# Kernel tuning notes

Measured on AMD Instinct MI355X. Metric: run time of the kernel, lower is better.

## Reference

```python
import jax, jax.numpy as jnp
import numpy as np

N_NODES = 50000
N_EDGES = 600000
NUM_GRAPHS = 64


def gcn_conv(x, W, b, src, dst, n):
    # PyG GCNConv: x' = D^{-1/2} (A + I) D^{-1/2} (x W) + b, self-loops implicit
    h = x @ W  # [N, H]
    deg = jax.ops.segment_sum(jnp.ones((src.shape[0],), h.dtype), dst, num_segments=n) + 1.0
    dinv = jax.lax.rsqrt(deg)  # [N]
    norm = dinv[src] * dinv[dst]  # [E]
    msg = h[src] * norm[:, None]  # [E, H] gather + scale
    agg = jax.ops.segment_sum(msg, dst, num_segments=n)  # scatter-add
    agg = agg + h * (dinv * dinv)[:, None]  # self-loop contribution
    return agg + b


def global_mean_pool(x, batch, num_graphs):
    s = jax.ops.segment_sum(x, batch, num_segments=num_graphs)
    cnt = jax.ops.segment_sum(jnp.ones((x.shape[0],), x.dtype), batch, num_segments=num_graphs)
    return s / jnp.maximum(cnt, 1.0)[:, None]


def setup_inputs() -> dict:
    key = jax.random.key(0)
    ks = jax.random.split(key, 12)
    x = jax.random.normal(ks[0], (N_NODES, 128), jnp.float32)
    edge_index = jax.random.randint(ks[1], (2, N_EDGES), 0, N_NODES, jnp.int64)
    batch = jnp.sort(jax.random.randint(ks[2], (N_NODES,), 0, NUM_GRAPHS, jnp.int64))
    W1 = jax.random.normal(ks[3], (128, 128), jnp.float32) * 0.08
    b1 = jax.random.normal(ks[4], (128,), jnp.float32) * 0.02
    W2 = jax.random.normal(ks[5], (128, 128), jnp.float32) * 0.08
    b2 = jax.random.normal(ks[6], (128,), jnp.float32) * 0.02
    Wfc1 = jax.random.normal(ks[7], (128, 64), jnp.float32) * 0.08
    bfc1 = jax.random.normal(ks[8], (64,), jnp.float32) * 0.02
    Wfc2 = jax.random.normal(ks[9], (64, 1), jnp.float32) * 0.08
    bfc2 = jax.random.normal(ks[10], (1,), jnp.float32) * 0.02
    return {"x": x, "edge_index": edge_index, "batch": batch,
            "W1": W1, "b1": b1, "W2": W2, "b2": b2,
            "Wfc1": Wfc1, "bfc1": bfc1, "Wfc2": Wfc2, "bfc2": bfc2}


def reference(x, edge_index, batch, W1, b1, W2, b2, Wfc1, bfc1, Wfc2, bfc2):
    n = x.shape[0]
    src, dst = edge_index[0], edge_index[1]
    h = jax.nn.relu(gcn_conv(x, W1, b1, src, dst, n))
    # dropout = identity (eval mode)
    h = jax.nn.relu(gcn_conv(h, W2, b2, src, dst, n))
    g = global_mean_pool(h, batch, NUM_GRAPHS)  # [G, H]
    g = jax.nn.relu(g @ Wfc1 + bfc1)
    return g @ Wfc2 + bfc2  # [G, 1]
```

## Files before the change

kernel.cpp:

```cpp
#include <hip/hip_runtime.h>
#include <hip/hip_fp16.h>


#define ELLK 40

typedef short bf16x8 __attribute__((ext_vector_type(8)));
typedef float f32x4  __attribute__((ext_vector_type(4)));

__device__ inline unsigned short f2bf_rne(float f) {
    unsigned u = __float_as_uint(f);
    unsigned r = (u + 0x7fffu + ((u >> 16) & 1u)) >> 16;
    return (unsigned short)r;
}
__device__ inline float bf2f(unsigned short h) {
    return __uint_as_float(((unsigned)h) << 16);
}

__global__ __launch_bounds__(256) void wconv_zero(const float* __restrict__ W1,
                                                  const float* __restrict__ W2,
                                                  unsigned short* __restrict__ W1h,
                                                  unsigned short* __restrict__ W1l,
                                                  unsigned short* __restrict__ W2h,
                                                  unsigned short* __restrict__ W2l,
                                                  int* __restrict__ count,
                                                  float* __restrict__ pooled,
                                                  float* __restrict__ cnt, int N) {
    int tid = threadIdx.x;
    int b = blockIdx.x;
    if (b < 128) {
        int i = b * 256 + tid;
        const float* W = (i < 16384) ? W1 : W2;
        unsigned short* Wh = (i < 16384) ? W1h : W2h;
        unsigned short* Wl = (i < 16384) ? W1l : W2l;
        int ii = i & 16383;
        int k = ii >> 7, n = ii & 127;
        float v = W[ii];
        unsigned short h = f2bf_rne(v);
        float lo = v - bf2f(h);
        int ct = n >> 4, nn = n & 15, ks = k >> 5, q = (k >> 3) & 3, j = k & 7;
        int oidx = (((ct * 4 + ks) * 64) + (q * 16 + nn)) * 8 + j;
        Wh[oidx] = h;
        Wl[oidx] = f2bf_rne(lo);
    } else {
        int idx = (b - 128) * 256 + tid;
        if (idx < N) count[idx] = 0;
        else if (idx < N + 8192) pooled[idx - N] = 0.f;
        else if (idx < N + 8256) cnt[idx - N - 8192] = 0.f;
    }
}

template <bool RELU_IN>
__device__ __forceinline__ void gemm_body(const float* __restrict__ X,
                                          const unsigned short* __restrict__ Wfh,
                                          const unsigned short* __restrict__ Wfl,
                                          __half* __restrict__ OUT, int M, int blk) {
    __shared__ unsigned short Xh[64][136];
    __shared__ unsigned short Xl[64][136];
    int tid = threadIdx.x;
    int w = tid >> 6, l = tid & 63;
    int m0 = blk * 64;

#pragma unroll
    for (int it = 0; it < 8; it++) {
        int i = tid + it * 256;
        int row = i >> 5, c4 = i & 31;
        int grow = m0 + row;
        float4 v = make_float4(0.f, 0.f, 0.f, 0.f);
        if (grow < M) v = *(const float4*)(X + (size_t)grow * 128 + c4 * 4);
        if (RELU_IN) {
            v.x = fmaxf(v.x, 0.f); v.y = fmaxf(v.y, 0.f);
            v.z = fmaxf(v.z, 0.f); v.w = fmaxf(v.w, 0.f);
        }
        float a[4] = {v.x, v.y, v.z, v.w};
        ushort4 hi, lo;
        unsigned short* hp = (unsigned short*)&hi;
        unsigned short* lp = (unsigned short*)&lo;
#pragma unroll
        for (int e = 0; e < 4; e++) {
            unsigned short h = f2bf_rne(a[e]);
            hp[e] = h;
            lp[e] = f2bf_rne(a[e] - bf2f(h));
        }
        *(ushort4*)&Xh[row][c4 * 4] = hi;
        *(ushort4*)&Xl[row][c4 * 4] = lo;
    }
    __syncthreads();

    int q = l >> 4, nn = l & 15;
    f32x4 acc[8];
#pragma unroll
    for (int ct = 0; ct < 8; ct++) acc[ct] = (f32x4){0.f, 0.f, 0.f, 0.f};

#pragma unroll
    for (int ks = 0; ks < 4; ks++) {
        bf16x8 ahi = *(const bf16x8*)&Xh[w * 16 + nn][ks * 32 + q * 8];
        bf16x8 alo = *(const bf16x8*)&Xl[w * 16 + nn][ks * 32 + q * 8];
#pragma unroll
        for (int ct = 0; ct < 8; ct++) {
            size_t fo = ((size_t)(ct * 4 + ks) * 64 + l) * 8;
            bf16x8 bhi = *(const bf16x8*)(Wfh + fo);
            bf16x8 blo = *(const bf16x8*)(Wfl + fo);
            acc[ct] = __builtin_amdgcn_mfma_f32_16x16x32_bf16(ahi, bhi, acc[ct], 0, 0, 0);
            acc[ct] = __builtin_amdgcn_mfma_f32_16x16x32_bf16(alo, bhi, acc[ct], 0, 0, 0);
            acc[ct] = __builtin_amdgcn_mfma_f32_16x16x32_bf16(ahi, blo, acc[ct], 0, 0, 0);
        }
    }
    __syncthreads();

#pragma unroll
    for (int r = 0; r < 4; r++) {
        int lrow = w * 16 + q * 4 + r;
#pragma unroll
        for (int ct = 0; ct < 8; ct++) {
            __half hv = __float2half(acc[ct][r]);
            Xh[lrow][ct * 16 + nn] = __half_as_ushort(hv);
        }
    }
    __syncthreads();
#pragma unroll
    for (int t = 0; t < 4; t++) {
        int c = tid + t * 256;
        int row = c >> 4, seg = c & 15;
        int grow = m0 + row;
        if (grow < M) {
            uint4 v = *(uint4*)&Xh[row][seg * 8];
            *(uint4*)((unsigned short*)OUT + (size_t)grow * 128 + seg * 8) = v;
        }
    }
}

__global__ __launch_bounds__(256) void gemm_mfma_relu(const float* __restrict__ X,
                                                      const unsigned short* __restrict__ Wfh,
                                                      const unsigned short* __restrict__ Wfl,
                                                      __half* __restrict__ OUT, int M) {
    gemm_body<true>(X, Wfh, Wfl, OUT, M, blockIdx.x);
}

__global__ __launch_bounds__(256) void fused_hg(const float* __restrict__ X,
                                                const unsigned short* __restrict__ Wfh,
                                                const unsigned short* __restrict__ Wfl,
                                                __half* __restrict__ OUT, int M, int gblocks,
                                                const int* __restrict__ dst,
                                                int* __restrict__ count,
                                                unsigned short* __restrict__ rank, int E) {
    if ((int)blockIdx.x < gblocks) {
        gemm_body<false>(X, Wfh, Wfl, OUT, M, blockIdx.x);
    } else {
        int e = ((int)blockIdx.x - gblocks) * 256 + (int)threadIdx.x;
        if (e < E) {
            int d = dst[e];
            rank[e] = (unsigned short)atomicAdd(&count[d], 1);
        }
    }
}

__global__ void scatter_norm(const int* __restrict__ src, const int* __restrict__ dst,
                             const unsigned short* __restrict__ rank,
                             const int* __restrict__ count,
                             int2* __restrict__ ell, int E) {
    int e = blockIdx.x * blockDim.x + threadIdx.x;
    if (e < E) {
        int s = src[e], d = dst[e];
        int r = rank[e];
        float ds = 1.0f / sqrtf((float)count[s] + 1.0f);
        float dd = 1.0f / sqrtf((float)count[d] + 1.0f);
        if (r < ELLK) ell[(size_t)d * ELLK + r] = make_int2(s, __float_as_int(ds * dd));
    }
}

__global__ __launch_bounds__(256) void gather_ell(const __half* __restrict__ h,
                                                  const float* __restrict__ bias,
                                                  const int* __restrict__ count,
                                                  const long long* __restrict__ ell,
                                                  float* __restrict__ B, int N) {
    int n = blockIdx.x * 4 + (threadIdx.x >> 6);
    int lane = threadIdx.x & 63;
    if (n >= N) return;
    int sub = lane >> 4, cl = lane & 15;
    int cn = count[n];
    int cnl = min(cn, ELLK);
    float din = 1.0f / sqrtf((float)cn + 1.0f);
    const unsigned short* hb = (const unsigned short*)h;
    const long long* row = ell + (size_t)n * ELLK;

    float a0 = 0.f, a1 = 0.f, a2 = 0.f, a3 = 0.f;
    float a4 = 0.f, a5 = 0.f, a6 = 0.f, a7 = 0.f;

    if (sub == 0) {
        float sw = din * din;
        uint4 raw = *(const uint4*)(hb + (size_t)n * 128 + cl * 8);
        const __half2* hh = (const __half2*)&raw;
        float2 f0 = __half22float2(hh[0]);
        float2 f1 = __half22float2(hh[1]);
        float2 f2 = __half22float2(hh[2]);
        float2 f3 = __half22float2(hh[3]);
        a0 = fmaf(f0.x, sw, a0); a1 = fmaf(f0.y, sw, a1);
        a2 = fmaf(f1.x, sw, a2); a3 = fmaf(f1.y, sw, a3);
        a4 = fmaf(f2.x, sw, a4); a5 = fmaf(f2.y, sw, a5);
        a6 = fmaf(f3.x, sw, a6); a7 = fmaf(f3.y, sw, a7);
    }

    for (int base = 0; base < cnl; base += 32) {
        int e1 = cnl - 1;
        long long v[8];
#pragma unroll
        for (int k = 0; k < 8; k++) {
            int j = base + sub + k * 4;
            v[k] = row[min(j, e1)];
        }
        float nr[8];
#pragma unroll
        for (int k = 0; k < 8; k++) {
            int j = base + sub + k * 4;
            nr[k] = (j < cnl) ? __int_as_float((int)(v[k] >> 32)) : 0.f;
        }
        uint4 r[8];
#pragma unroll
        for (int k = 0; k < 8; k++)
            r[k] = *(const uint4*)(hb + (size_t)(int)v[k] * 128 + cl * 8);
#pragma unroll
        for (int k = 0; k < 8; k++) {
            const __half2* hh = (const __half2*)&r[k];
            float2 f0 = __half22float2(hh[0]), f1 = __half22float2(hh[1]);
            float2 f2 = __half22float2(hh[2]), f3 = __half22float2(hh[3]);
            a0 = fmaf(f0.x, nr[k], a0); a1 = fmaf(f0.y, nr[k], a1);
            a2 = fmaf(f1.x, nr[k], a2); a3 = fmaf(f1.y, nr[k], a3);
            a4 = fmaf(f2.x, nr[k], a4); a5 = fmaf(f2.y, nr[k], a5);
            a6 = fmaf(f3.x, nr[k], a6); a7 = fmaf(f3.y, nr[k], a7);
        }
    }

#pragma unroll
    for (int m = 16; m < 64; m <<= 1) {
        a0 += __shfl_xor(a0, m, 64); a1 += __shfl_xor(a1, m, 64);
        a2 += __shfl_xor(a2, m, 64); a3 += __shfl_xor(a3, m, 64);
        a4 += __shfl_xor(a4, m, 64); a5 += __shfl_xor(a5, m, 64);
        a6 += __shfl_xor(a6, m, 64); a7 += __shfl_xor(a7, m, 64);
    }

    if (sub == 0) {
        float4 o0, o1;
        o0.x = a0 + bias[cl * 8 + 0]; o0.y = a1 + bias[cl * 8 + 1];
        o0.z = a2 + bias[cl * 8 + 2]; o0.w = a3 + bias[cl * 8 + 3];
        o1.x = a4 + bias[cl * 8 + 4]; o1.y = a5 + bias[cl * 8 + 5];
        o1.z = a6 + bias[cl * 8 + 6]; o1.w = a7 + bias[cl * 8 + 7];
        *(float4*)(B + (size_t)n * 128 + cl * 8) = o0;
        *(float4*)(B + (size_t)n * 128 + cl * 8 + 4) = o1;
    }
}

__global__ __launch_bounds__(256) void pool_kernel(const float* __restrict__ B,
                                                   const int* __restrict__ batch,
                                                   float* pooled, float* cnt, int N) {
    int c = threadIdx.x & 127;
    int half = threadIdx.x >> 7;
    int n0 = blockIdx.x * 128;
    float acc = 0.f, cacc = 0.f;
    int curg = -1;
    for (int i = half; i < 128; i += 2) {
        int n = n0 + i;
        if (n >= N) break;
        int g = batch[n];
        float v = fmaxf(B[(size_t)n * 128 + c], 0.f);
        if (g != curg) {
            if (curg >= 0) {
                atomicAdd(&pooled[curg * 128 + c], acc);
                if (c == 0) atomicAdd(&cnt[curg], cacc);
            }
            curg = g; acc = 0.f; cacc = 0.f;
        }
        acc += v; cacc += 1.f;
    }
    if (curg >= 0) {
        atomicAdd(&pooled[curg * 128 + c], acc);
        if (c == 0) atomicAdd(&cnt[curg], cacc);
    }
}

__global__ __launch_bounds__(64) void head_kernel(const float* __restrict__ pooled,
                                                  const float* __restrict__ cnt,
                                                  const float* __restrict__ Wfc1,
                                                  const float* __restrict__ bfc1,
                                                  const float* __restrict__ Wfc2,
                                                  const float* __restrict__ bfc2,
                                                  float* __restrict__ out) {
    __shared__ float mean[128];
    int g = blockIdx.x;
    int t = threadIdx.x;
    float inv = 1.0f / fmaxf(cnt[g], 1.0f);
    mean[t] = pooled[g * 128 + t] * inv;
    mean[t + 64] = pooled[g * 128 + t + 64] * inv;
    __syncthreads();
    float s = bfc1[t];
#pragma unroll 4
    for (int k = 0; k < 128; k++) s = fmaf(mean[k], Wfc1[k * 64 + t], s);
    float p = fmaxf(s, 0.f) * Wfc2[t];
#pragma unroll
    for (int o = 32; o > 0; o >>= 1) p += __shfl_down(p, o, 64);
    if (t == 0) out[g] = p + bfc2[0];
}

extern "C" void kernel_launch(void* const* d_in, const int* in_sizes, int n_in,
                              void* d_out, int out_size, void* d_ws, size_t ws_size,
                              hipStream_t stream) {
    const float* x    = (const float*)d_in[0];
    const int*   edge = (const int*)d_in[1];
    const int*   batch= (const int*)d_in[2];
    const float* W1   = (const float*)d_in[3];
    const float* b1   = (const float*)d_in[4];
    const float* W2   = (const float*)d_in[5];
    const float* b2   = (const float*)d_in[6];
    const float* Wfc1 = (const float*)d_in[7];
    const float* bfc1 = (const float*)d_in[8];
    const float* Wfc2 = (const float*)d_in[9];
    const float* bfc2 = (const float*)d_in[10];
    float* out = (float*)d_out;

    int N = in_sizes[0] / 128;
    int E = in_sizes[1] / 2;
    const int* src = edge;
    const int* dst = edge + E;

    char* ws = (char*)d_ws;
    size_t off = 0;
    auto alloc = [&](size_t bytes) { void* p = ws + off; off += (bytes + 255) & ~(size_t)255; return p; };
    __half* Ah    = (__half*)alloc((size_t)N * 128 * sizeof(__half));
    float* B      = (float*)alloc((size_t)N * 128 * sizeof(float));
    int*   count  = (int*)alloc((size_t)N * sizeof(int));
    unsigned short* rank = (unsigned short*)alloc((size_t)E * sizeof(unsigned short));
    int2*  ell    = (int2*)alloc((size_t)N * ELLK * sizeof(int2));
    float* pooled = (float*)alloc(64 * 128 * sizeof(float));
    float* cnt    = (float*)alloc(64 * sizeof(float));
    unsigned short* W1h = (unsigned short*)alloc(16384 * sizeof(short));
    unsigned short* W1l = (unsigned short*)alloc(16384 * sizeof(short));
    unsigned short* W2h = (unsigned short*)alloc(16384 * sizeof(short));
    unsigned short* W2l = (unsigned short*)alloc(16384 * sizeof(short));

    int hb = (E + 255) / 256;
    int gblocks = (N + 63) / 64;
    int ablocks = (N + 3) / 4;
    int zb = (N + 8256 + 255) / 256;

    wconv_zero<<<128 + zb, 256, 0, stream>>>(W1, W2, W1h, W1l, W2h, W2l,
                                             count, pooled, cnt, N);

    fused_hg<<<gblocks + hb, 256, 0, stream>>>(x, W1h, W1l, Ah, N, gblocks,
                                               dst, count, rank, E);

    scatter_norm<<<hb, 256, 0, stream>>>(src, dst, rank, count, ell, E);

    gather_ell<<<ablocks, 256, 0, stream>>>(Ah, b1, count, (const long long*)ell, B, N);

    gemm_mfma_relu<<<gblocks, 256, 0, stream>>>(B, W2h, W2l, Ah, N);

    gather_ell<<<ablocks, 256, 0, stream>>>(Ah, b2, count, (const long long*)ell, B, N);

    pool_kernel<<<(N + 127) / 128, 256, 0, stream>>>(B, batch, pooled, cnt, N);
    head_kernel<<<64, 64, 0, stream>>>(pooled, cnt, Wfc1, bfc1, Wfc2, bfc2, out);
}
```

Before: 259.2 us.

## Fuse layer-1 aggregation with layer-2 GEMM and layer-2 aggregation with pooling

Replaces four kernels (gather, relu-GEMM, gather, pool) with two. The first applies bias and ReLU to the aggregated rows, splits them into bf16 hi/lo halves in shared memory and runs the MFMA GEMM in the same block. The second aggregates and mean-pools from shared memory. This drops the fp32 intermediate buffer round trips through HBM and two launches. In exchange, the gather unroll falls from 8 to 4 edges per subgroup, which lowers memory-level parallelism, and the 512-thread blocks use more shared memory, which can lower occupancy.

```diff
diff --git a/kernel.cpp b/kernel.cpp
--- a/kernel.cpp
+++ b/kernel.cpp
@@ -129,13 +129,6 @@
     }
 }
 
-__global__ __launch_bounds__(256) void gemm_mfma_relu(const float* __restrict__ X,
-                                                      const unsigned short* __restrict__ Wfh,
-                                                      const unsigned short* __restrict__ Wfl,
-                                                      __half* __restrict__ OUT, int M) {
-    gemm_body<true>(X, Wfh, Wfl, OUT, M, blockIdx.x);
-}
-
 __global__ __launch_bounds__(256) void fused_hg(const float* __restrict__ X,
                                                 const unsigned short* __restrict__ Wfh,
                                                 const unsigned short* __restrict__ Wfl,
@@ -168,100 +161,208 @@
     }
 }
 
-__global__ __launch_bounds__(256) void gather_ell(const __half* __restrict__ h,
-                                                  const float* __restrict__ bias,
-                                                  const int* __restrict__ count,
-                                                  const long long* __restrict__ ell,
-                                                  float* __restrict__ B, int N) {
-    int n = blockIdx.x * 4 + (threadIdx.x >> 6);
-    int lane = threadIdx.x & 63;
-    if (n >= N) return;
-    int sub = lane >> 4, cl = lane & 15;
+__device__ __forceinline__ void gather_node(const unsigned short* __restrict__ hb,
+                                            const long long* __restrict__ ell,
+                                            const int* __restrict__ count,
+                                            int n, int sub, int cl, float a[8]) {
     int cn = count[n];
     int cnl = min(cn, ELLK);
     float din = 1.0f / sqrtf((float)cn + 1.0f);
-    const unsigned short* hb = (const unsigned short*)h;
     const long long* row = ell + (size_t)n * ELLK;
-
-    float a0 = 0.f, a1 = 0.f, a2 = 0.f, a3 = 0.f;
-    float a4 = 0.f, a5 = 0.f, a6 = 0.f, a7 = 0.f;
-
     if (sub == 0) {
         float sw = din * din;
         uint4 raw = *(const uint4*)(hb + (size_t)n * 128 + cl * 8);
         const __half2* hh = (const __half2*)&raw;
-        float2 f0 = __half22float2(hh[0]);
-        float2 f1 = __half22float2(hh[1]);
-        float2 f2 = __half22float2(hh[2]);
-        float2 f3 = __half22float2(hh[3]);
-        a0 = fmaf(f0.x, sw, a0); a1 = fmaf(f0.y, sw, a1);
-        a2 = fmaf(f1.x, sw, a2); a3 = fmaf(f1.y, sw, a3);
-        a4 = fmaf(f2.x, sw, a4); a5 = fmaf(f2.y, sw, a5);
-        a6 = fmaf(f3.x, sw, a6); a7 = fmaf(f3.y, sw, a7);
-    }
-
-    for (int base = 0; base < cnl; base += 32) {
+        float2 f0 = __half22float2(hh[0]), f1 = __half22float2(hh[1]);
+        float2 f2 = __half22float2(hh[2]), f3 = __half22float2(hh[3]);
+        a[0] = fmaf(f0.x, sw, a[0]); a[1] = fmaf(f0.y, sw, a[1]);
+        a[2] = fmaf(f1.x, sw, a[2]); a[3] = fmaf(f1.y, sw, a[3]);
+        a[4] = fmaf(f2.x, sw, a[4]); a[5] = fmaf(f2.y, sw, a[5]);
+        a[6] = fmaf(f3.x, sw, a[6]); a[7] = fmaf(f3.y, sw, a[7]);
+    }
+    for (int base = 0; base < cnl; base += 16) {
         int e1 = cnl - 1;
-        long long v[8];
-#pragma unroll
-        for (int k = 0; k < 8; k++) {
-            int j = base + sub + k * 4;
-            v[k] = row[min(j, e1)];
-        }
-        float nr[8];
-#pragma unroll
-        for (int k = 0; k < 8; k++) {
-            int j = base + sub + k * 4;
-            nr[k] = (j < cnl) ? __int_as_float((int)(v[k] >> 32)) : 0.f;
-        }
-        uint4 r[8];
-#pragma unroll
-        for (int k = 0; k < 8; k++)
-            r[k] = *(const uint4*)(hb + (size_t)(int)v[k] * 128 + cl * 8);
-#pragma unroll
-        for (int k = 0; k < 8; k++) {
-            const __half2* hh = (const __half2*)&r[k];
+        int j0 = base + sub, j1 = j0 + 4, j2 = j0 + 8, j3 = j0 + 12;
+        long long v0 = row[min(j0, e1)];
+        long long v1 = row[min(j1, e1)];
+        long long v2 = row[min(j2, e1)];
+        long long v3 = row[min(j3, e1)];
+        float n0 = (j0 < cnl) ? __int_as_float((int)(v0 >> 32)) : 0.f;
+        float n1 = (j1 < cnl) ? __int_as_float((int)(v1 >> 32)) : 0.f;
+        float n2 = (j2 < cnl) ? __int_as_float((int)(v2 >> 32)) : 0.f;
+        float n3 = (j3 < cnl) ? __int_as_float((int)(v3 >> 32)) : 0.f;
+        uint4 r0 = *(const uint4*)(hb + (size_t)(int)v0 * 128 + cl * 8);
+        uint4 r1 = *(const uint4*)(hb + (size_t)(int)v1 * 128 + cl * 8);
+        uint4 r2 = *(const uint4*)(hb + (size_t)(int)v2 * 128 + cl * 8);
+        uint4 r3 = *(const uint4*)(hb + (size_t)(int)v3 * 128 + cl * 8);
+        {
+            const __half2* hh = (const __half2*)&r0;
             float2 f0 = __half22float2(hh[0]), f1 = __half22float2(hh[1]);
             float2 f2 = __half22float2(hh[2]), f3 = __half22float2(hh[3]);
-            a0 = fmaf(f0.x, nr[k], a0); a1 = fmaf(f0.y, nr[k], a1);
-            a2 = fmaf(f1.x, nr[k], a2); a3 = fmaf(f1.y, nr[k], a3);
-            a4 = fmaf(f2.x, nr[k], a4); a5 = fmaf(f2.y, nr[k], a5);
-            a6 = fmaf(f3.x, nr[k], a6); a7 = fmaf(f3.y, nr[k], a7);
-        }
-    }
-
-#pragma unroll
-    for (int m = 16; m < 64; m <<= 1) {
-        a0 += __shfl_xor(a0, m, 64); a1 += __shfl_xor(a1, m, 64);
-        a2 += __shfl_xor(a2, m, 64); a3 += __shfl_xor(a3, m, 64);
-        a4 += __shfl_xor(a4, m, 64); a5 += __shfl_xor(a5, m, 64);
-        a6 += __shfl_xor(a6, m, 64); a7 += __shfl_xor(a7, m, 64);
-    }
-
-    if (sub == 0) {
-        float4 o0, o1;
-        o0.x = a0 + bias[cl * 8 + 0]; o0.y = a1 + bias[cl * 8 + 1];
-        o0.z = a2 + bias[cl * 8 + 2]; o0.w = a3 + bias[cl * 8 + 3];
-        o1.x = a4 + bias[cl * 8 + 4]; o1.y = a5 + bias[cl * 8 + 5];
-        o1.z = a6 + bias[cl * 8 + 6]; o1.w = a7 + bias[cl * 8 + 7];
-        *(float4*)(B + (size_t)n * 128 + cl * 8) = o0;
-        *(float4*)(B + (size_t)n * 128 + cl * 8 + 4) = o1;
-    }
-}
-
-__global__ __launch_bounds__(256) void pool_kernel(const float* __restrict__ B,
+            a[0] = fmaf(f0.x, n0, a[0]); a[1] = fmaf(f0.y, n0, a[1]);
+            a[2] = fmaf(f1.x, n0, a[2]); a[3] = fmaf(f1.y, n0, a[3]);
+            a[4] = fmaf(f2.x, n0, a[4]); a[5] = fmaf(f2.y, n0, a[5]);
+            a[6] = fmaf(f3.x, n0, a[6]); a[7] = fmaf(f3.y, n0, a[7]);
+        }
+        {
+            const __half2* hh = (const __half2*)&r1;
+            float2 f0 = __half22float2(hh[0]), f1 = __half22float2(hh[1]);
+            float2 f2 = __half22float2(hh[2]), f3 = __half22float2(hh[3]);
+            a[0] = fmaf(f0.x, n1, a[0]); a[1] = fmaf(f0.y, n1, a[1]);
+            a[2] = fmaf(f1.x, n1, a[2]); a[3] = fmaf(f1.y, n1, a[3]);
+            a[4] = fmaf(f2.x, n1, a[4]); a[5] = fmaf(f2.y, n1, a[5]);
+            a[6] = fmaf(f3.x, n1, a[6]); a[7] = fmaf(f3.y, n1, a[7]);
+        }
+        {
+            const __half2* hh = (const __half2*)&r2;
+            float2 f0 = __half22float2(hh[0]), f1 = __half22float2(hh[1]);
+            float2 f2 = __half22float2(hh[2]), f3 = __half22float2(hh[3]);
+            a[0] = fmaf(f0.x, n2, a[0]); a[1] = fmaf(f0.y, n2, a[1]);
+            a[2] = fmaf(f1.x, n2, a[2]); a[3] = fmaf(f1.y, n2, a[3]);
+            a[4] = fmaf(f2.x, n2, a[4]); a[5] = fmaf(f2.y, n2, a[5]);
+            a[6] = fmaf(f3.x, n2, a[6]); a[7] = fmaf(f3.y, n2, a[7]);
+        }
+        {
+            const __half2* hh = (const __half2*)&r3;
+            float2 f0 = __half22float2(hh[0]), f1 = __half22float2(hh[1]);
+            float2 f2 = __half22float2(hh[2]), f3 = __half22float2(hh[3]);
+            a[0] = fmaf(f0.x, n3, a[0]); a[1] = fmaf(f0.y, n3, a[1]);
+            a[2] = fmaf(f1.x, n3, a[2]); a[3] = fmaf(f1.y, n3, a[3]);
+            a[4] = fmaf(f2.x, n3, a[4]); a[5] = fmaf(f2.y, n3, a[5]);
+            a[6] = fmaf(f3.x, n3, a[6]); a[7] = fmaf(f3.y, n3, a[7]);
+        }
+    }
+}
+
+__global__ __launch_bounds__(512) void gather_gemm(const __half* __restrict__ h,
+                                                   const float* __restrict__ bias,
+                                                   const int* __restrict__ count,
+                                                   const long long* __restrict__ ell,
+                                                   const unsigned short* __restrict__ Wfh,
+                                                   const unsigned short* __restrict__ Wfl,
+                                                   __half* __restrict__ OUT, int N) {
+    __shared__ unsigned short Xh[64][136];
+    __shared__ unsigned short Xl[64][136];
+    int tid = threadIdx.x;
+    int w = tid >> 6, l = tid & 63;
+    int sub = l >> 4, cl = l & 15;
+    int m0 = blockIdx.x * 64;
+    const unsigned short* hb = (const unsigned short*)h;
+
+    for (int rr = 0; rr < 8; rr++) {
+        int lrow = w * 8 + rr;
+        int n = m0 + lrow;
+        float a[8] = {0.f, 0.f, 0.f, 0.f, 0.f, 0.f, 0.f, 0.f};
+        if (n < N) gather_node(hb, ell, count, n, sub, cl, a);
+#pragma unroll
+        for (int m = 16; m < 64; m <<= 1) {
+#pragma unroll
+            for (int k = 0; k < 8; k++) a[k] += __shfl_xor(a[k], m, 64);
+        }
+        if (sub == 0) {
+            unsigned short hs[8], ls[8];
+#pragma unroll
+            for (int k = 0; k < 8; k++) {
+                float v = fmaxf(a[k] + bias[cl * 8 + k], 0.f);
+                unsigned short hh = f2bf_rne(v);
+                hs[k] = hh;
+                ls[k] = f2bf_rne(v - bf2f(hh));
+            }
+            *(ushort4*)&Xh[lrow][cl * 8]     = *(ushort4*)&hs[0];
+            *(ushort4*)&Xh[lrow][cl * 8 + 4] = *(ushort4*)&hs[4];
+            *(ushort4*)&Xl[lrow][cl * 8]     = *(ushort4*)&ls[0];
+            *(ushort4*)&Xl[lrow][cl * 8 + 4] = *(ushort4*)&ls[4];
+        }
+    }
+    __syncthreads();
+
+    int q = l >> 4, nn = l & 15;
+    int w2 = w & 3;
+    int ch = (w >> 2) * 4;
+    f32x4 acc[4];
+#pragma unroll
+    for (int ct2 = 0; ct2 < 4; ct2++) acc[ct2] = (f32x4){0.f, 0.f, 0.f, 0.f};
+#pragma unroll
+    for (int ks = 0; ks < 4; ks++) {
+        bf16x8 ahi = *(const bf16x8*)&Xh[w2 * 16 + nn][ks * 32 + q * 8];
+        bf16x8 alo = *(const bf16x8*)&Xl[w2 * 16 + nn][ks * 32 + q * 8];
+#pragma unroll
+        for (int ct2 = 0; ct2 < 4; ct2++) {
+            int ct = ch + ct2;
+            size_t fo = ((size_t)(ct * 4 + ks) * 64 + l) * 8;
+            bf16x8 bhi = *(const bf16x8*)(Wfh + fo);
+            bf16x8 blo = *(const bf16x8*)(Wfl + fo);
+            acc[ct2] = __builtin_amdgcn_mfma_f32_16x16x32_bf16(ahi, bhi, acc[ct2], 0, 0, 0);
+            acc[ct2] = __builtin_amdgcn_mfma_f32_16x16x32_bf16(alo, bhi, acc[ct2], 0, 0, 0);
+            acc[ct2] = __builtin_amdgcn_mfma_f32_16x16x32_bf16(ahi, blo, acc[ct2], 0, 0, 0);
+        }
+    }
+    __syncthreads();
+#pragma unroll
+    for (int r = 0; r < 4; r++) {
+        int lrow = w2 * 16 + q * 4 + r;
+#pragma unroll
+        for (int ct2 = 0; ct2 < 4; ct2++) {
+            __half hv = __float2half(acc[ct2][r]);
+            Xh[lrow][(ch + ct2) * 16 + nn] = __half_as_ushort(hv);
+        }
+    }
+    __syncthreads();
+#pragma unroll
+    for (int t = 0; t < 2; t++) {
+        int c = tid + t * 512;
+        int row = c >> 4, seg = c & 15;
+        int grow = m0 + row;
+        if (grow < N) {
+            uint4 v = *(uint4*)&Xh[row][seg * 8];
+            *(uint4*)((unsigned short*)OUT + (size_t)grow * 128 + seg * 8) = v;
+        }
+    }
+}
+
+__global__ __launch_bounds__(512) void gather_pool(const __half* __restrict__ h,
+                                                   const float* __restrict__ bias,
+                                                   const int* __restrict__ count,
+                                                   const long long* __restrict__ ell,
                                                    const int* __restrict__ batch,
-                                                   float* pooled, float* cnt, int N) {
-    int c = threadIdx.x & 127;
-    int half = threadIdx.x >> 7;
-    int n0 = blockIdx.x * 128;
+                                                   float* __restrict__ pooled,
+                                                   float* __restrict__ cnt, int N) {
+    __shared__ float P[64][128];
+    __shared__ int gb[64];
+    int tid = threadIdx.x;
+    int w = tid >> 6, l = tid & 63;
+    int sub = l >> 4, cl = l & 15;
+    int m0 = blockIdx.x * 64;
+    const unsigned short* hb = (const unsigned short*)h;
+
+    if (tid < 64) gb[tid] = (m0 + tid < N) ? batch[m0 + tid] : -1;
+
+    for (int rr = 0; rr < 8; rr++) {
+        int lrow = w * 8 + rr;
+        int n = m0 + lrow;
+        float a[8] = {0.f, 0.f, 0.f, 0.f, 0.f, 0.f, 0.f, 0.f};
+        if (n < N) gather_node(hb, ell, count, n, sub, cl, a);
+#pragma unroll
+        for (int m = 16; m < 64; m <<= 1) {
+#pragma unroll
+            for (int k = 0; k < 8; k++) a[k] += __shfl_xor(a[k], m, 64);
+        }
+        if (sub == 0 && n < N) {
+#pragma unroll
+            for (int k = 0; k < 8; k++)
+                P[lrow][cl * 8 + k] = fmaxf(a[k] + bias[cl * 8 + k], 0.f);
+        }
+    }
+    __syncthreads();
+
+    int c = tid & 127, quarter = tid >> 7;
     float acc = 0.f, cacc = 0.f;
     int curg = -1;
-    for (int i = half; i < 128; i += 2) {
-        int n = n0 + i;
+    for (int i = quarter * 16; i < quarter * 16 + 16; i++) {
+        int n = m0 + i;
         if (n >= N) break;
-        int g = batch[n];
-        float v = fmaxf(B[(size_t)n * 128 + c], 0.f);
+        int g = gb[i];
+        float v = P[i][c];
         if (g != curg) {
             if (curg >= 0) {
                 atomicAdd(&pooled[curg * 128 + c], acc);
@@ -325,7 +426,7 @@
     size_t off = 0;
     auto alloc = [&](size_t bytes) { void* p = ws + off; off += (bytes + 255) & ~(size_t)255; return p; };
     __half* Ah    = (__half*)alloc((size_t)N * 128 * sizeof(__half));
-    float* B      = (float*)alloc((size_t)N * 128 * sizeof(float));
+    __half* Ah2   = (__half*)alloc((size_t)N * 128 * sizeof(__half));
     int*   count  = (int*)alloc((size_t)N * sizeof(int));
     unsigned short* rank = (unsigned short*)alloc((size_t)E * sizeof(unsigned short));
     int2*  ell    = (int2*)alloc((size_t)N * ELLK * sizeof(int2));
@@ -338,7 +439,7 @@
 
     int hb = (E + 255) / 256;
     int gblocks = (N + 63) / 64;
-    int ablocks = (N + 3) / 4;
+    int fblocks = (N + 63) / 64;
     int zb = (N + 8256 + 255) / 256;
 
     wconv_zero<<<128 + zb, 256, 0, stream>>>(W1, W2, W1h, W1l, W2h, W2l,
@@ -349,12 +450,11 @@
 
     scatter_norm<<<hb, 256, 0, stream>>>(src, dst, rank, count, ell, E);
 
-    gather_ell<<<ablocks, 256, 0, stream>>>(Ah, b1, count, (const long long*)ell, B, N);
-
-    gemm_mfma_relu<<<gblocks, 256, 0, stream>>>(B, W2h, W2l, Ah, N);
-
-    gather_ell<<<ablocks, 256, 0, stream>>>(Ah, b2, count, (const long long*)ell, B, N);
-
-    pool_kernel<<<(N + 127) / 128, 256, 0, stream>>>(B, batch, pooled, cnt, N);
+    gather_gemm<<<fblocks, 512, 0, stream>>>(Ah, b1, count, (const long long*)ell,
+                                             W2h, W2l, Ah2, N);
+
+    gather_pool<<<fblocks, 512, 0, stream>>>(Ah2, b2, count, (const long long*)ell,
+                                             batch, pooled, cnt, N);
+
     head_kernel<<<64, 64, 0, stream>>>(pooled, cnt, Wfc1, bfc1, Wfc2, bfc2, out);
 }
```

New measurement: 238.9 us. -7.8%, faster.
